# Kernel tuning notes

Measured on AMD Instinct MI355X. Metric: run time of the kernel, lower is better.

## Reference

```python
import jax, jax.numpy as jnp
import numpy as np

N_USER, N_IMG, N_TXT = 100000, 100000, 100000
E = 800000
IN_C, OUT_C = 256, 128


def setup_inputs() -> dict:
    key = jax.random.key(0)
    ks = jax.random.split(key, 12)
    inp = {
        "x_user": jax.random.normal(ks[0], (N_USER, IN_C), jnp.float32),
        "x_image": jax.random.normal(ks[1], (N_IMG, OUT_C), jnp.float32),
        "x_text": jax.random.normal(ks[2], (N_TXT, OUT_C), jnp.float32),
        "edge_img": jax.random.randint(ks[3], (2, E), 0, N_USER, jnp.int64),
        "edge_txt": jax.random.randint(ks[4], (2, E), 0, N_USER, jnp.int64),
        # user_linear params
        "W_user": jax.random.normal(ks[5], (IN_C, OUT_C), jnp.float32) / np.sqrt(IN_C),
        "b_user": jnp.zeros((OUT_C,), jnp.float32),
        # SAGEConv image->user: lin_l (neighbors, with bias), lin_r (root, no bias)
        "Wl_img": jax.random.normal(ks[6], (OUT_C, OUT_C), jnp.float32) / np.sqrt(OUT_C),
        "bl_img": jnp.zeros((OUT_C,), jnp.float32),
        "Wr_img": jax.random.normal(ks[7], (OUT_C, OUT_C), jnp.float32) / np.sqrt(OUT_C),
        # SAGEConv text->user
        "Wl_txt": jax.random.normal(ks[8], (OUT_C, OUT_C), jnp.float32) / np.sqrt(OUT_C),
        "bl_txt": jnp.zeros((OUT_C,), jnp.float32),
        "Wr_txt": jax.random.normal(ks[9], (OUT_C, OUT_C), jnp.float32) / np.sqrt(OUT_C),
    }
    return inp


def _sage(x_src, edge, Wl, bl, Wr, x_dst):
    # SAGEConv (mean aggr): out = lin_l(mean_{j in N(i)} x_j) + lin_r(x_i)
    src, dst = edge[0], edge[1]
    n_dst = x_dst.shape[0]
    msg = x_src[src]                                   # [E, C] gather
    agg = jax.ops.segment_sum(msg, dst, num_segments=n_dst)  # [N, C] scatter-add
    cnt = jax.ops.segment_sum(jnp.ones((edge.shape[1], 1), x_src.dtype), dst,
                              num_segments=n_dst)
    mean = agg / jnp.maximum(cnt, 1.0)                 # nodes w/o edges -> 0
    return mean @ Wl + bl + x_dst @ Wr


def reference(x_user, x_image, x_text, edge_img, edge_txt,
              W_user, b_user, Wl_img, bl_img, Wr_img, Wl_txt, bl_txt, Wr_txt):
    u = x_user @ W_user + b_user                       # user_linear
    out_img = _sage(x_image, edge_img, Wl_img, bl_img, Wr_img, u)
    out_txt = _sage(x_text, edge_txt, Wl_txt, bl_txt, Wr_txt, u)
    # HeteroConv default aggr='sum' over relations, then ReLU
    return jax.nn.relu(out_img + out_txt)
```

## Files before the change

### kernel.cpp

```cpp
#include <hip/hip_runtime.h>


#define BK 4096
#define MAXBUK 256

typedef __attribute__((ext_vector_type(8))) short bf16x8;
typedef __attribute__((ext_vector_type(8))) unsigned short u16x8;
typedef __attribute__((ext_vector_type(4))) float f32x4;
typedef __attribute__((ext_vector_type(2))) float f32x2;

__device__ __forceinline__ ushort f2b(float x) {
    union { float f; unsigned u; } v; v.f = x;
    unsigned r = (v.u + 0x7FFF + ((v.u >> 16) & 1)) >> 16;
    return (ushort)r;
}
__device__ __forceinline__ float b2f(ushort u) {
    union { unsigned u; float f; } v; v.u = (unsigned)u << 16;
    return v.f;
}
__device__ __forceinline__ void acc4(unsigned w, float* a) {
    f32x2 lo = __builtin_amdgcn_cvt_pk_f32_fp8((int)w, false);
    f32x2 hi = __builtin_amdgcn_cvt_pk_f32_fp8((int)w, true);
    a[0] += lo[0]; a[1] += lo[1]; a[2] += hi[0]; a[3] += hi[1];
}

__global__ __launch_bounds__(256) void k_front(
        const float* __restrict__ x_image, const float* __restrict__ x_text,
        const int* __restrict__ edge_i, const int* __restrict__ edge_t,
        const float* __restrict__ Wl_i, const float* __restrict__ Wl_t,
        const float* __restrict__ W_user, const float* __restrict__ b_user,
        const float* __restrict__ Wr_i, const float* __restrict__ Wr_t,
        const float* __restrict__ bl_i, const float* __restrict__ bl_t,
        unsigned char* __restrict__ xib, unsigned char* __restrict__ xtb,
        ushort* __restrict__ Bp, float* __restrict__ bias,
        int* __restrict__ counts,
        int N, int E, int nblkR, int nbuk, int nbP) {
    __shared__ int h[MAXBUK];
    const int bid = blockIdx.x;
    const int tid = threadIdx.x;
    const int NBLK = 2 * nblkR;

    if (bid < nbP) {
        int i = bid * 256 + tid;
        int j = i & 7, lane = (i >> 3) & 63, cf = (i >> 9) & 7, ks = i >> 12;
        int kk = ks * 32 + (lane >> 4) * 8 + j;
        int col = cf * 16 + (lane & 15);
        float v;
        if (kk < 128)      v = Wl_i[kk * 128 + col];
        else if (kk < 256) v = Wl_t[(kk - 128) * 128 + col];
        else {
            int k2 = kk - 256;
            float s = 0.f;
            for (int c1 = 0; c1 < 128; ++c1)
                s += W_user[k2 * 128 + c1] * (Wr_i[c1 * 128 + col] + Wr_t[c1 * 128 + col]);
            v = s;
        }
        Bp[i] = f2b(v);
        if (i < 128) {
            float b = bl_i[i] + bl_t[i];
            for (int k2 = 0; k2 < 128; ++k2)
                b += b_user[k2] * (Wr_i[k2 * 128 + i] + Wr_t[k2 * 128 + i]);
            bias[i] = b;
        }
    } else if (bid < nbP + NBLK) {
        int hb = bid - nbP;
        int rel = (hb >= nblkR) ? 1 : 0;
        int blk = hb - rel * nblkR;
        const int* eg = rel ? edge_t : edge_i;
        const int relN = rel * N;
        for (int i = tid; i < nbuk; i += 256) h[i] = 0;
        __syncthreads();
        int base = blk * BK;
        #pragma unroll
        for (int j = 0; j < 4; ++j) {
            int e = base + (j * 256 + tid) * 4;
            if (e + 3 < E) {
                int4 d4 = *reinterpret_cast<const int4*>(eg + E + e);
                atomicAdd(&h[(relN + d4.x) >> 10], 1);
                atomicAdd(&h[(relN + d4.y) >> 10], 1);
                atomicAdd(&h[(relN + d4.z) >> 10], 1);
                atomicAdd(&h[(relN + d4.w) >> 10], 1);
            } else {
                for (int q = 0; q < 4; ++q) {
                    int ee = e + q;
                    if (ee < E) atomicAdd(&h[(relN + eg[E + ee]) >> 10], 1);
                }
            }
        }
        __syncthreads();
        for (int i = tid; i < nbuk; i += 256) counts[(size_t)hb * nbuk + i] = h[i];
    } else {
        int t = (bid - nbP - NBLK) * 256 + tid;
        int n8 = N * 16;
        if (t >= 2 * n8) return;
        int relc = (t >= n8) ? 1 : 0;
        const float* src = relc ? x_text : x_image;
        unsigned char* dst = relc ? xtb : xib;
        int i = relc ? t - n8 : t;
        float4 f0 = *reinterpret_cast<const float4*>(src + (size_t)i * 8);
        float4 f1 = *reinterpret_cast<const float4*>(src + (size_t)i * 8 + 4);
        int w0 = 0, w1 = 0;
        w0 = __builtin_amdgcn_cvt_pk_fp8_f32(f0.x, f0.y, w0, false);
        w0 = __builtin_amdgcn_cvt_pk_fp8_f32(f0.z, f0.w, w0, true);
        w1 = __builtin_amdgcn_cvt_pk_fp8_f32(f1.x, f1.y, w1, false);
        w1 = __builtin_amdgcn_cvt_pk_fp8_f32(f1.z, f1.w, w1, true);
        *reinterpret_cast<uint2*>(dst + (size_t)i * 8) = make_uint2((unsigned)w0, (unsigned)w1);
    }
}

__global__ __launch_bounds__(256) void k_s1(int* __restrict__ counts,
                                            int* __restrict__ T,
                                            int NBLK, int nbuk) {
    __shared__ int a[512];
    __shared__ int ps[256];
    const int b = blockIdx.x, t = threadIdx.x;
    a[t]       = (t < NBLK)       ? counts[(size_t)t * nbuk + b] : 0;
    a[t + 256] = (t + 256 < NBLK) ? counts[(size_t)(t + 256) * nbuk + b] : 0;
    __syncthreads();
    int x0 = a[2 * t], x1 = a[2 * t + 1];
    int s = x0 + x1;
    ps[t] = s; __syncthreads();
    for (int off = 1; off < 256; off <<= 1) {
        int add = (t >= off) ? ps[t - off] : 0;
        __syncthreads();
        ps[t] += add;
        __syncthreads();
    }
    int ex = ps[t] - s;
    if (2 * t < NBLK)     counts[(size_t)(2 * t) * nbuk + b] = ex;
    if (2 * t + 1 < NBLK) counts[(size_t)(2 * t + 1) * nbuk + b] = ex + x0;
    if (t == 255) T[b] = ps[255];
}

__global__ __launch_bounds__(256) void k_s2(const int* __restrict__ T,
                                            int* __restrict__ Bb,
                                            int* __restrict__ rowptr,
                                            int M, int Etot, int nbuk) {
    __shared__ int sh[256];
    int t = threadIdx.x;
    int v = (t < nbuk) ? T[t] : 0;
    sh[t] = v; __syncthreads();
    for (int off = 1; off < 256; off <<= 1) {
        int add = (t >= off) ? sh[t - off] : 0;
        __syncthreads();
        sh[t] += add;
        __syncthreads();
    }
    if (t < nbuk) Bb[t] = sh[t] - v;
    if (t == 0) { Bb[nbuk] = Etot; rowptr[M] = Etot; }
}

__global__ __launch_bounds__(512) void k_part1(
        const int* __restrict__ edge_i, const int* __restrict__ edge_t,
        const int* __restrict__ counts, const int* __restrict__ Bb,
        unsigned* __restrict__ pairs, int N, int E, int nblkR, int nbuk) {
    __shared__ int cur[MAXBUK];
    const int bid = blockIdx.x, tid = threadIdx.x;
    int rel = (bid >= nblkR) ? 1 : 0;
    int blk = bid - rel * nblkR;
    const int* eg = rel ? edge_t : edge_i;
    const int relN = rel * N;
    for (int i = tid; i < nbuk; i += 512)
        cur[i] = Bb[i] + counts[(size_t)bid * nbuk + i];
    __syncthreads();
    int base = blk * BK;
    #pragma unroll
    for (int j = 0; j < 2; ++j) {
        int e = base + (j * 512 + tid) * 4;
        if (e + 3 < E) {
            int4 d4 = *reinterpret_cast<const int4*>(eg + E + e);
            int4 s4 = *reinterpret_cast<const int4*>(eg + e);
            int k0 = relN + d4.x, k1 = relN + d4.y, k2 = relN + d4.z, k3 = relN + d4.w;
            int p0 = atomicAdd(&cur[k0 >> 10], 1);
            pairs[p0] = ((unsigned)(k0 & 1023) << 17) | (unsigned)s4.x;
            int p1 = atomicAdd(&cur[k1 >> 10], 1);
            pairs[p1] = ((unsigned)(k1 & 1023) << 17) | (unsigned)s4.y;
            int p2 = atomicAdd(&cur[k2 >> 10], 1);
            pairs[p2] = ((unsigned)(k2 & 1023) << 17) | (unsigned)s4.z;
            int p3 = atomicAdd(&cur[k3 >> 10], 1);
            pairs[p3] = ((unsigned)(k3 & 1023) << 17) | (unsigned)s4.w;
        } else {
            for (int q = 0; q < 4; ++q) {
                int ee = e + q;
                if (ee < E) {
                    int k0 = relN + eg[E + ee];
                    int p0 = atomicAdd(&cur[k0 >> 10], 1);
                    pairs[p0] = ((unsigned)(k0 & 1023) << 17) | (unsigned)eg[ee];
                }
            }
        }
    }
}

__global__ __launch_bounds__(512) void k_part2(
        const unsigned* __restrict__ pairs, const int* __restrict__ Bb,
        int* __restrict__ rowptr, int* __restrict__ col, int M) {
    __shared__ int h[1024];
    __shared__ int ps[512];
    const int b = blockIdx.x, t = threadIdx.x;
    const int key0 = b << 10;
    const int beg = Bb[b], end = Bb[b + 1];
    h[t] = 0; h[t + 512] = 0;
    __syncthreads();
    for (int p = beg + t; p < end; p += 512)
        atomicAdd(&h[pairs[p] >> 17], 1);
    __syncthreads();
    int v0 = h[2 * t], v1 = h[2 * t + 1];
    int s = v0 + v1;
    ps[t] = s; __syncthreads();
    for (int off = 1; off < 512; off <<= 1) {
        int add = (t >= off) ? ps[t - off] : 0;
        __syncthreads();
        ps[t] += add;
        __syncthreads();
    }
    int run = ps[t] - s + beg;
    __syncthreads();
    int k = key0 + 2 * t;
    if (k < M) rowptr[k] = run;
    h[2 * t] = run; run += v0;
    if (k + 1 < M) rowptr[k + 1] = run;
    h[2 * t + 1] = run;
    __syncthreads();
    for (int p = beg + t; p < end; p += 512) {
        unsigned pr = pairs[p];
        int slot = atomicAdd(&h[pr >> 17], 1);
        col[slot] = (int)(pr & 0x1FFFFu);
    }
}

__global__ __launch_bounds__(256) void k_gather_mean(
        const unsigned char* __restrict__ xib, const unsigned char* __restrict__ xtb,
        const int* __restrict__ rowptr, const int* __restrict__ col,
        ushort* __restrict__ mi, ushort* __restrict__ mt, int N) {
    int t = blockIdx.x * 256 + threadIdx.x;
    int node = t >> 3, lane = t & 7;
    if (node >= N) return;
    int rel = blockIdx.y;
    const unsigned char* xs = rel ? xtb : xib;
    ushort* mean = rel ? mt : mi;
    const int c0 = lane * 16;
    int rb = rel * N + node;
    int beg = rowptr[rb], end = rowptr[rb + 1];
    float a[16];
    #pragma unroll
    for (int q = 0; q < 16; ++q) a[q] = 0.f;
    int j = beg;
    for (; j + 3 < end; j += 4) {
        int s0 = col[j], s1 = col[j + 1], s2 = col[j + 2], s3 = col[j + 3];
        uint4 v0 = *reinterpret_cast<const uint4*>(xs + (size_t)s0 * 128 + c0);
        uint4 v1 = *reinterpret_cast<const uint4*>(xs + (size_t)s1 * 128 + c0);
        uint4 v2 = *reinterpret_cast<const uint4*>(xs + (size_t)s2 * 128 + c0);
        uint4 v3 = *reinterpret_cast<const uint4*>(xs + (size_t)s3 * 128 + c0);
        acc4(v0.x, a + 0); acc4(v0.y, a + 4); acc4(v0.z, a + 8); acc4(v0.w, a + 12);
        acc4(v1.x, a + 0); acc4(v1.y, a + 4); acc4(v1.z, a + 8); acc4(v1.w, a + 12);
        acc4(v2.x, a + 0); acc4(v2.y, a + 4); acc4(v2.z, a + 8); acc4(v2.w, a + 12);
        acc4(v3.x, a + 0); acc4(v3.y, a + 4); acc4(v3.z, a + 8); acc4(v3.w, a + 12);
    }
    for (; j < end; ++j) {
        uint4 v0 = *reinterpret_cast<const uint4*>(xs + (size_t)col[j] * 128 + c0);
        acc4(v0.x, a + 0); acc4(v0.y, a + 4); acc4(v0.z, a + 8); acc4(v0.w, a + 12);
    }
    float r = (end > beg) ? 1.0f / (float)(end - beg) : 0.0f;
    u16x8 o0, o1;
    #pragma unroll
    for (int q = 0; q < 8; ++q) { o0[q] = f2b(a[q] * r); o1[q] = f2b(a[q + 8] * r); }
    *reinterpret_cast<u16x8*>(mean + (size_t)node * 128 + c0) = o0;
    *reinterpret_cast<u16x8*>(mean + (size_t)node * 128 + c0 + 8) = o1;
}

__global__ __launch_bounds__(1024) void k_final_mfma(
        const ushort* __restrict__ mi, const ushort* __restrict__ mt,
        const float* __restrict__ x_user, const ushort* __restrict__ Bp,
        const float* __restrict__ bias, float* __restrict__ out, int N) {
    extern __shared__ u16x8 bl8[];
    const int tid = threadIdx.x;
    const int wid = tid >> 6, lane = tid & 63;
    const int r0g = blockIdx.x * 512 + wid * 32 + (lane & 15);
    const int rA0 = min(r0g, N - 1);
    const int rA1 = min(r0g + 16, N - 1);
    const int kh = (lane >> 4) * 8;
    f32x4 acc0[8] = {}, acc1[8] = {};

    const u16x8* Bp8 = reinterpret_cast<const u16x8*>(Bp);
    #pragma unroll
    for (int it = 0; it < 8; ++it)
        bl8[it * 1024 + tid] = Bp8[it * 1024 + tid];
    __syncthreads();

    #pragma unroll
    for (int ks = 0; ks < 8; ++ks) {
        const ushort* s = (ks < 4) ? mi : mt;
        bf16x8 a0 = *reinterpret_cast<const bf16x8*>(s + (size_t)rA0 * 128 + (ks & 3) * 32 + kh);
        bf16x8 a1 = *reinterpret_cast<const bf16x8*>(s + (size_t)rA1 * 128 + (ks & 3) * 32 + kh);
        #pragma unroll
        for (int cf = 0; cf < 8; ++cf) {
            bf16x8 bb = *reinterpret_cast<const bf16x8*>(&bl8[(ks * 8 + cf) * 64 + lane]);
            acc0[cf] = __builtin_amdgcn_mfma_f32_16x16x32_bf16(a0, bb, acc0[cf], 0, 0, 0);
            acc1[cf] = __builtin_amdgcn_mfma_f32_16x16x32_bf16(a1, bb, acc1[cf], 0, 0, 0);
        }
    }
    const float* Xr0 = x_user + (size_t)rA0 * 256;
    const float* Xr1 = x_user + (size_t)rA1 * 256;
    #pragma unroll
    for (int ks = 8; ks < 16; ++ks) {
        int k0 = (ks - 8) * 32 + kh;
        float4 f0 = *reinterpret_cast<const float4*>(Xr0 + k0);
        float4 f1 = *reinterpret_cast<const float4*>(Xr0 + k0 + 4);
        float4 g0 = *reinterpret_cast<const float4*>(Xr1 + k0);
        float4 g1 = *reinterpret_cast<const float4*>(Xr1 + k0 + 4);
        bf16x8 a0, a1;
        a0[0] = (short)f2b(f0.x); a0[1] = (short)f2b(f0.y);
        a0[2] = (short)f2b(f0.z); a0[3] = (short)f2b(f0.w);
        a0[4] = (short)f2b(f1.x); a0[5] = (short)f2b(f1.y);
        a0[6] = (short)f2b(f1.z); a0[7] = (short)f2b(f1.w);
        a1[0] = (short)f2b(g0.x); a1[1] = (short)f2b(g0.y);
        a1[2] = (short)f2b(g0.z); a1[3] = (short)f2b(g0.w);
        a1[4] = (short)f2b(g1.x); a1[5] = (short)f2b(g1.y);
        a1[6] = (short)f2b(g1.z); a1[7] = (short)f2b(g1.w);
        #pragma unroll
        for (int cf = 0; cf < 8; ++cf) {
            bf16x8 bb = *reinterpret_cast<const bf16x8*>(&bl8[(ks * 8 + cf) * 64 + lane]);
            acc0[cf] = __builtin_amdgcn_mfma_f32_16x16x32_bf16(a0, bb, acc0[cf], 0, 0, 0);
            acc1[cf] = __builtin_amdgcn_mfma_f32_16x16x32_bf16(a1, bb, acc1[cf], 0, 0, 0);
        }
    }

    const int col0 = lane & 15;
    const int rbase = blockIdx.x * 512 + wid * 32 + (lane >> 4) * 4;
    #pragma unroll
    for (int cf = 0; cf < 8; ++cf) {
        int c = cf * 16 + col0;
        float bv = bias[c];
        #pragma unroll
        for (int r = 0; r < 4; ++r) {
            int row = rbase + r;
            if (row < N) out[(size_t)row * 128 + c] = fmaxf(acc0[cf][r] + bv, 0.f);
            int row2 = rbase + 16 + r;
            if (row2 < N) out[(size_t)row2 * 128 + c] = fmaxf(acc1[cf][r] + bv, 0.f);
        }
    }
}

extern "C" void kernel_launch(void* const* d_in, const int* in_sizes, int n_in,
                              void* d_out, int out_size, void* d_ws, size_t ws_size,
                              hipStream_t stream) {
    const float* x_user  = (const float*)d_in[0];
    const float* x_image = (const float*)d_in[1];
    const float* x_text  = (const float*)d_in[2];
    const int*   edge_i  = (const int*)d_in[3];
    const int*   edge_t  = (const int*)d_in[4];
    const float* W_user  = (const float*)d_in[5];
    const float* b_user  = (const float*)d_in[6];
    const float* Wl_img  = (const float*)d_in[7];
    const float* bl_img  = (const float*)d_in[8];
    const float* Wr_img  = (const float*)d_in[9];
    const float* Wl_txt  = (const float*)d_in[10];
    const float* bl_txt  = (const float*)d_in[11];
    const float* Wr_txt  = (const float*)d_in[12];

    const int N = in_sizes[0] / 256;
    const int E = in_sizes[3] / 2;
    const int M = 2 * N;
    const int nblkR = (E + BK - 1) / BK;
    const int NBLK = 2 * nblkR;
    const int nbuk = (M + 1023) >> 10;

    unsigned char* xib = (unsigned char*)d_ws;
    unsigned char* xtb = xib + (size_t)N * 128;
    ushort*   mi     = (ushort*)(xtb + (size_t)N * 128);
    ushort*   mt     = mi + (size_t)N * 128;
    ushort*   Bp     = mt + (size_t)N * 128;
    float*    bias   = (float*)(Bp + 65536);
    int*      counts = (int*)(bias + 128);
    int*      T      = counts + (size_t)NBLK * nbuk;
    int*      Bb     = T + 256;
    int*      rowptr = Bb + 260;
    int*      col    = rowptr + (M + 4);
    unsigned* pairs  = (unsigned*)(col + (size_t)2 * E);

    const int nbP = 256;
    const int nbC = (2 * N * 16 + 255) / 256;
    k_front<<<nbP + NBLK + nbC, 256, 0, stream>>>(
        x_image, x_text, edge_i, edge_t,
        Wl_img, Wl_txt, W_user, b_user, Wr_img, Wr_txt, bl_img, bl_txt,
        xib, xtb, Bp, bias, counts, N, E, nblkR, nbuk, nbP);

    k_s1<<<nbuk, 256, 0, stream>>>(counts, T, NBLK, nbuk);
    k_s2<<<1, 256, 0, stream>>>(T, Bb, rowptr, M, 2 * E, nbuk);
    k_part1<<<NBLK, 512, 0, stream>>>(edge_i, edge_t, counts, Bb, pairs,
                                      N, E, nblkR, nbuk);
    k_part2<<<nbuk, 512, 0, stream>>>(pairs, Bb, rowptr, col, M);

    {
        dim3 g((N * 8 + 255) / 256, 2);
        k_gather_mean<<<g, 256, 0, stream>>>(xib, xtb, rowptr, col, mi, mt, N);
    }

    k_final_mfma<<<(N + 511) / 512, 1024, 131072, stream>>>(
        mi, mt, x_user, Bp, bias, (float*)d_out, N);
}
```

Before: 158.8 us.

## Fold bucket scan into partition kernels and halve final GEMM tile footprint

Measured after the change: 152.6 us. 1.04x faster.

```diff
diff --git a/kernel.cpp b/kernel.cpp
--- a/kernel.cpp
+++ b/kernel.cpp
@@ -132,37 +132,30 @@
     if (t == 255) T[b] = ps[255];
 }
 
-__global__ __launch_bounds__(256) void k_s2(const int* __restrict__ T,
-                                            int* __restrict__ Bb,
-                                            int* __restrict__ rowptr,
-                                            int M, int Etot, int nbuk) {
-    __shared__ int sh[256];
-    int t = threadIdx.x;
-    int v = (t < nbuk) ? T[t] : 0;
-    sh[t] = v; __syncthreads();
-    for (int off = 1; off < 256; off <<= 1) {
-        int add = (t >= off) ? sh[t - off] : 0;
-        __syncthreads();
-        sh[t] += add;
-        __syncthreads();
-    }
-    if (t < nbuk) Bb[t] = sh[t] - v;
-    if (t == 0) { Bb[nbuk] = Etot; rowptr[M] = Etot; }
-}
-
 __global__ __launch_bounds__(512) void k_part1(
         const int* __restrict__ edge_i, const int* __restrict__ edge_t,
-        const int* __restrict__ counts, const int* __restrict__ Bb,
+        const int* __restrict__ counts, const int* __restrict__ T,
         unsigned* __restrict__ pairs, int N, int E, int nblkR, int nbuk) {
     __shared__ int cur[MAXBUK];
+    __shared__ int ps[256];
     const int bid = blockIdx.x, tid = threadIdx.x;
+    int v = 0;
+    if (tid < 256) { v = (tid < nbuk) ? T[tid] : 0; ps[tid] = v; }
+    __syncthreads();
+    for (int off = 1; off < 256; off <<= 1) {
+        int add = (tid >= off && tid < 256) ? ps[tid - off] : 0;
+        __syncthreads();
+        if (tid < 256) ps[tid] += add;
+        __syncthreads();
+    }
+    if (tid < nbuk)
+        cur[tid] = (ps[tid] - v) + counts[(size_t)bid * nbuk + tid];
+    __syncthreads();
+
     int rel = (bid >= nblkR) ? 1 : 0;
     int blk = bid - rel * nblkR;
     const int* eg = rel ? edge_t : edge_i;
     const int relN = rel * N;
-    for (int i = tid; i < nbuk; i += 512)
-        cur[i] = Bb[i] + counts[(size_t)bid * nbuk + i];
-    __syncthreads();
     int base = blk * BK;
     #pragma unroll
     for (int j = 0; j < 2; ++j) {
@@ -193,13 +186,27 @@
 }
 
 __global__ __launch_bounds__(512) void k_part2(
-        const unsigned* __restrict__ pairs, const int* __restrict__ Bb,
-        int* __restrict__ rowptr, int* __restrict__ col, int M) {
+        const unsigned* __restrict__ pairs, const int* __restrict__ T,
+        int* __restrict__ rowptr, int* __restrict__ col, int M, int nbuk) {
     __shared__ int h[1024];
     __shared__ int ps[512];
+    __shared__ int s_beg, s_end;
     const int b = blockIdx.x, t = threadIdx.x;
     const int key0 = b << 10;
-    const int beg = Bb[b], end = Bb[b + 1];
+    int v = 0;
+    if (t < 256) { v = (t < nbuk) ? T[t] : 0; ps[t] = v; }
+    __syncthreads();
+    for (int off = 1; off < 256; off <<= 1) {
+        int add = (t >= off && t < 256) ? ps[t - off] : 0;
+        __syncthreads();
+        if (t < 256) ps[t] += add;
+        __syncthreads();
+    }
+    if (t == b) { s_beg = ps[b] - v; s_end = ps[b]; }
+    if (b == 0 && t == nbuk - 1) rowptr[M] = ps[nbuk - 1];
+    __syncthreads();
+    const int beg = s_beg, end = s_end;
+
     h[t] = 0; h[t + 512] = 0;
     __syncthreads();
     for (int p = beg + t; p < end; p += 512)
@@ -273,61 +280,56 @@
         const ushort* __restrict__ mi, const ushort* __restrict__ mt,
         const float* __restrict__ x_user, const ushort* __restrict__ Bp,
         const float* __restrict__ bias, float* __restrict__ out, int N) {
-    extern __shared__ u16x8 bl8[];
+    __shared__ u16x8 bl8[4096];
     const int tid = threadIdx.x;
     const int wid = tid >> 6, lane = tid & 63;
-    const int r0g = blockIdx.x * 512 + wid * 32 + (lane & 15);
+    const int r0g = blockIdx.x * 256 + wid * 16 + (lane & 15);
     const int rA0 = min(r0g, N - 1);
-    const int rA1 = min(r0g + 16, N - 1);
     const int kh = (lane >> 4) * 8;
-    f32x4 acc0[8] = {}, acc1[8] = {};
+    f32x4 acc[8] = {};
 
     const u16x8* Bp8 = reinterpret_cast<const u16x8*>(Bp);
-    #pragma unroll
-    for (int it = 0; it < 8; ++it)
+
+    #pragma unroll
+    for (int it = 0; it < 4; ++it)
         bl8[it * 1024 + tid] = Bp8[it * 1024 + tid];
     __syncthreads();
-
     #pragma unroll
     for (int ks = 0; ks < 8; ++ks) {
         const ushort* s = (ks < 4) ? mi : mt;
         bf16x8 a0 = *reinterpret_cast<const bf16x8*>(s + (size_t)rA0 * 128 + (ks & 3) * 32 + kh);
-        bf16x8 a1 = *reinterpret_cast<const bf16x8*>(s + (size_t)rA1 * 128 + (ks & 3) * 32 + kh);
         #pragma unroll
         for (int cf = 0; cf < 8; ++cf) {
             bf16x8 bb = *reinterpret_cast<const bf16x8*>(&bl8[(ks * 8 + cf) * 64 + lane]);
-            acc0[cf] = __builtin_amdgcn_mfma_f32_16x16x32_bf16(a0, bb, acc0[cf], 0, 0, 0);
-            acc1[cf] = __builtin_amdgcn_mfma_f32_16x16x32_bf16(a1, bb, acc1[cf], 0, 0, 0);
-        }
-    }
+            acc[cf] = __builtin_amdgcn_mfma_f32_16x16x32_bf16(a0, bb, acc[cf], 0, 0, 0);
+        }
+    }
+    __syncthreads();
+
+    #pragma unroll
+    for (int it = 0; it < 4; ++it)
+        bl8[it * 1024 + tid] = Bp8[4096 + it * 1024 + tid];
+    __syncthreads();
     const float* Xr0 = x_user + (size_t)rA0 * 256;
-    const float* Xr1 = x_user + (size_t)rA1 * 256;
-    #pragma unroll
-    for (int ks = 8; ks < 16; ++ks) {
-        int k0 = (ks - 8) * 32 + kh;
+    #pragma unroll
+    for (int ks = 0; ks < 8; ++ks) {
+        int k0 = ks * 32 + kh;
         float4 f0 = *reinterpret_cast<const float4*>(Xr0 + k0);
         float4 f1 = *reinterpret_cast<const float4*>(Xr0 + k0 + 4);
-        float4 g0 = *reinterpret_cast<const float4*>(Xr1 + k0);
-        float4 g1 = *reinterpret_cast<const float4*>(Xr1 + k0 + 4);
-        bf16x8 a0, a1;
+        bf16x8 a0;
         a0[0] = (short)f2b(f0.x); a0[1] = (short)f2b(f0.y);
         a0[2] = (short)f2b(f0.z); a0[3] = (short)f2b(f0.w);
         a0[4] = (short)f2b(f1.x); a0[5] = (short)f2b(f1.y);
         a0[6] = (short)f2b(f1.z); a0[7] = (short)f2b(f1.w);
-        a1[0] = (short)f2b(g0.x); a1[1] = (short)f2b(g0.y);
-        a1[2] = (short)f2b(g0.z); a1[3] = (short)f2b(g0.w);
-        a1[4] = (short)f2b(g1.x); a1[5] = (short)f2b(g1.y);
-        a1[6] = (short)f2b(g1.z); a1[7] = (short)f2b(g1.w);
         #pragma unroll
         for (int cf = 0; cf < 8; ++cf) {
             bf16x8 bb = *reinterpret_cast<const bf16x8*>(&bl8[(ks * 8 + cf) * 64 + lane]);
-            acc0[cf] = __builtin_amdgcn_mfma_f32_16x16x32_bf16(a0, bb, acc0[cf], 0, 0, 0);
-            acc1[cf] = __builtin_amdgcn_mfma_f32_16x16x32_bf16(a1, bb, acc1[cf], 0, 0, 0);
+            acc[cf] = __builtin_amdgcn_mfma_f32_16x16x32_bf16(a0, bb, acc[cf], 0, 0, 0);
         }
     }
 
     const int col0 = lane & 15;
-    const int rbase = blockIdx.x * 512 + wid * 32 + (lane >> 4) * 4;
+    const int rbase = blockIdx.x * 256 + wid * 16 + (lane >> 4) * 4;
     #pragma unroll
     for (int cf = 0; cf < 8; ++cf) {
         int c = cf * 16 + col0;
@@ -335,9 +337,7 @@
         #pragma unroll
         for (int r = 0; r < 4; ++r) {
             int row = rbase + r;
-            if (row < N) out[(size_t)row * 128 + c] = fmaxf(acc0[cf][r] + bv, 0.f);
-            int row2 = rbase + 16 + r;
-            if (row2 < N) out[(size_t)row2 * 128 + c] = fmaxf(acc1[cf][r] + bv, 0.f);
+            if (row < N) out[(size_t)row * 128 + c] = fmaxf(acc[cf][r] + bv, 0.f);
         }
     }
 }
@@ -374,8 +374,7 @@
     float*    bias   = (float*)(Bp + 65536);
     int*      counts = (int*)(bias + 128);
     int*      T      = counts + (size_t)NBLK * nbuk;
-    int*      Bb     = T + 256;
-    int*      rowptr = Bb + 260;
+    int*      rowptr = T + 256;
     int*      col    = rowptr + (M + 4);
     unsigned* pairs  = (unsigned*)(col + (size_t)2 * E);
 
@@ -387,16 +386,15 @@
         xib, xtb, Bp, bias, counts, N, E, nblkR, nbuk, nbP);
 
     k_s1<<<nbuk, 256, 0, stream>>>(counts, T, NBLK, nbuk);
-    k_s2<<<1, 256, 0, stream>>>(T, Bb, rowptr, M, 2 * E, nbuk);
-    k_part1<<<NBLK, 512, 0, stream>>>(edge_i, edge_t, counts, Bb, pairs,
+    k_part1<<<NBLK, 512, 0, stream>>>(edge_i, edge_t, counts, T, pairs,
                                       N, E, nblkR, nbuk);
-    k_part2<<<nbuk, 512, 0, stream>>>(pairs, Bb, rowptr, col, M);
+    k_part2<<<nbuk, 512, 0, stream>>>(pairs, T, rowptr, col, M, nbuk);
 
     {
         dim3 g((N * 8 + 255) / 256, 2);
         k_gather_mean<<<g, 256, 0, stream>>>(xib, xtb, rowptr, col, mi, mt, N);
     }
 
-    k_final_mfma<<<(N + 511) / 512, 1024, 131072, stream>>>(
+    k_final_mfma<<<(N + 255) / 256, 1024, 0, stream>>>(
         mi, mt, x_user, Bp, bias, (float*)d_out, N);
 }
```
